# Performance work log

Hardware: AMD Instinct MI355X
Metric: run time of the kernel (lower is better)

Reference implementation:

```python
import jax, jax.numpy as jnp
import numpy as np


def lstm(xs, Wk, Wr, b, return_seq):
    # xs: (B, T, Din); Keras gate order i, f, c(g), o
    B = xs.shape[0]
    H = Wr.shape[0]

    def step(carry, x_t):
        h, c = carry
        z = x_t @ Wk + h @ Wr + b  # (B, 4H)
        i, f, g, o = jnp.split(z, 4, axis=-1)
        i = jax.nn.sigmoid(i)
        f = jax.nn.sigmoid(f)
        g = jnp.tanh(g)
        o = jax.nn.sigmoid(o)
        c = f * c + i * g
        h = o * jnp.tanh(c)
        return (h, c), h

    h0 = jnp.zeros((B, H), xs.dtype)
    (h, _), hs = jax.lax.scan(step, (h0, h0), jnp.swapaxes(xs, 0, 1))
    return jnp.swapaxes(hs, 0, 1) if return_seq else h


def setup_inputs() -> dict:
    key = jax.random.key(0)
    ks = jax.random.split(key, 10)
    B, T, F, H, P, O = 8192, 20, 8, 256, 15, 2
    s = 0.05
    return {
        "x": jax.random.normal(ks[0], (B, T, F), jnp.float32),
        "w_in_k": jax.random.normal(ks[1], (F, 64), jnp.float32) * s,
        "w_in_b": jnp.zeros((64,), jnp.float32),
        "enc_k": jax.random.normal(ks[2], (64, 4 * H), jnp.float32) * s,
        "enc_rk": jax.random.normal(ks[3], (H, 4 * H), jnp.float32) * s,
        "enc_b": jnp.zeros((4 * H,), jnp.float32),
        "dec_k": jax.random.normal(ks[4], (H, 4 * H), jnp.float32) * s,
        "dec_rk": jax.random.normal(ks[5], (H, 4 * H), jnp.float32) * s,
        "dec_b": jnp.zeros((4 * H,), jnp.float32),
        "mean_k": jax.random.normal(ks[6], (H, O), jnp.float32) * s,
        "mean_b": jnp.zeros((O,), jnp.float32),
        "lv_k": jax.random.normal(ks[7], (H, O), jnp.float32) * s,
        "lv_b": jnp.zeros((O,), jnp.float32),
    }


def reference(x, w_in_k, w_in_b, enc_k, enc_rk, enc_b,
              dec_k, dec_rk, dec_b, mean_k, mean_b, lv_k, lv_b):
    NUM_PRED = 15
    # input projection: Dense(64, relu)
    h = jax.nn.relu(x @ w_in_k + w_in_b)          # (B, T, 64)
    enc = lstm(h, enc_k, enc_rk, enc_b, False)    # (B, 256) last state
    rep = jnp.repeat(enc[:, None, :], NUM_PRED, axis=1)  # RepeatVector
    dec = lstm(rep, dec_k, dec_rk, dec_b, True)   # (B, 15, 256)
    mean = dec @ mean_k + mean_b                  # (B, 15, 2)
    log_var = jax.nn.relu(dec @ lv_k + lv_b)      # (B, 15, 2)
    return jnp.concatenate([mean, log_var], axis=-1)  # (B, 15, 4)
```

## Files before the change

kernel.cpp:

```cpp
#include <hip/hip_runtime.h>

#define TT 20
#define FF 8
#define HH 256
#define PP 15
#define DP 64
#define ROWS 32
#define NTHR 512
#define NBLK 256

typedef __attribute__((ext_vector_type(8))) _Float16 hfrag;
typedef __attribute__((ext_vector_type(16))) float f32x16;
typedef __attribute__((ext_vector_type(4))) float f32x4;

__device__ __forceinline__ int sw(int row, int k, int w){
  return (row * w + k) ^ ((row & 7) << 3);
}
__device__ __forceinline__ f32x16 zero16(){
  f32x16 v;
  #pragma unroll
  for (int i = 0; i < 16; ++i) v[i] = 0.f;
  return v;
}

__global__ void wprep(const float* __restrict__ ek, const float* __restrict__ erk,
                      const float* __restrict__ dk, const float* __restrict__ drk,
                      _Float16* __restrict__ ws){
  int i = blockIdx.x * 256 + threadIdx.x;
  const float* src; _Float16* dst; int ksh, rel;
  if (i < 4096)        { src = ek;  ksh = 2; rel = i;          dst = ws;           }
  else if (i < 20480)  { src = erk; ksh = 4; rel = i - 4096;   dst = ws + 65536;   }
  else if (i < 36864)  { src = dk;  ksh = 4; rel = i - 20480;  dst = ws + 327680;  }
  else                 { src = drk; ksh = 4; rel = i - 36864;  dst = ws + 589824;  }
  int lcol = rel & 31;
  int gkc  = rel >> 5;
  int kc   = gkc & ((1 << ksh) - 1);
  int wg   = gkc >> ksh;
  int g    = wg & 3, wid = wg >> 2;
  int col  = g * 256 + wid * 32 + lcol;
  int base = gkc * 512;
  #pragma unroll
  for (int lkh = 0; lkh < 2; ++lkh){
    _Float16 hbuf[8];
    #pragma unroll
    for (int e = 0; e < 8; ++e){
      int k = kc * 16 + lkh * 8 + e;
      hbuf[e] = (_Float16)src[k * 1024 + col];
    }
    int off = base + (lkh * 32 + lcol) * 8;
    *reinterpret_cast<hfrag*>(&dst[off]) = *reinterpret_cast<hfrag*>(hbuf);
  }
}

#define MM_STEPA(ACC, HSRC, WT, KD, NKC)                                                     \
  { const _Float16* ph = (WT) + (wid * 4 * (NKC)) * 512 + lane * 8;                          \
    _Pragma("unroll 4")                                                                      \
    for (int kc = 0; kc < (NKC); ++kc){                                                      \
      int k0 = kc * 16 + lkh * 8;                                                            \
      hfrag a = *reinterpret_cast<const hfrag*>(&(HSRC)[sw(lcol, k0, (KD))]);                \
      _Pragma("unroll")                                                                      \
      for (int g = 0; g < 4; ++g){                                                           \
        hfrag b = *reinterpret_cast<const hfrag*>(ph + (g * (NKC) + kc) * 512);              \
        ACC[g] = __builtin_amdgcn_mfma_f32_32x32x16_f16(a, b, ACC[g], 0, 0, 0);              \
      }                                                                                      \
    }                                                                                        \
  }

#define GATE_UPDATE(HDST, B0, B1, B2, B3, DOZERO)                                            \
  { _Pragma("unroll")                                                                        \
    for (int rg = 0; rg < 16; ++rg){                                                         \
      float zi = acc[0][rg] + (B0);                                                          \
      float zf = acc[1][rg] + (B1);                                                          \
      float zg = acc[2][rg] + (B2);                                                          \
      float zo = acc[3][rg] + (B3);                                                          \
      float ei = __expf(-zi), ef = __expf(-zf), eo = __expf(-zo);                            \
      float eg = __expf(2.f * zg);                                                           \
      float r1 = __builtin_amdgcn_rcpf(1.f + ef);                                            \
      float r2 = __builtin_amdgcn_rcpf((1.f + ei) * (eg + 1.f));                             \
      float cv = cst[rg] * r1 + (eg - 1.f) * r2;                        \
      cst[rg] = cv;                                                                          \
      float ec = __expf(2.f * cv);                                                           \
      float r3 = __builtin_amdgcn_rcpf((1.f + eo) * (ec + 1.f));                             \
      float hv = (ec - 1.f) * r3;                                             \
      int row = (rg & 3) + 8 * (rg >> 2) + 4 * lkh;                                          \
      (HDST)[sw(row, j, HH)] = (_Float16)hv;                                                 \
    }                                                                                        \
    if (DOZERO){ _Pragma("unroll") for (int g = 0; g < 4; ++g) acc[g] = zero16(); }          \
  }

#define STAGE_XP(tt, buf)                                                                    \
  { _Pragma("unroll")                                                                        \
    for (int rr = 0; rr < 4; ++rr){                                                          \
      int row = rb + 8 * rr;                                                                 \
      const float* xr = x + ((long)(r0 + row) * TT + (tt)) * FF;                             \
      f32x4 xa = *reinterpret_cast<const f32x4*>(xr);                                        \
      f32x4 xv = *reinterpret_cast<const f32x4*>(xr + 4);                                    \
      float s = bwin;                                                                        \
      _Pragma("unroll")                                                                      \
      for (int f = 0; f < 4; ++f){                                                           \
        s += xa[f] * winK[f * DP + xc];                                                      \
        s += xv[f] * winK[(f + 4) * DP + xc];                                                \
      }                                                                                      \
      s = fmaxf(s, 0.f);                                                                     \
      xb[buf][sw(row, xc, DP)] = (_Float16)s;                                                \
    } }

#define OUT_HEAD(tt)                                                                         \
  { float s = 0.f;                                                                           \
    _Pragma("unroll")                                                                        \
    for (int kb = 0; kb < 8; ++kb){                                                          \
      int k0 = sub_o * 64 + kb * 8;                                                          \
      hfrag vh = *reinterpret_cast<const hfrag*>(&h2[sw(orow_o, k0, HH)]);                   \
      _Pragma("unroll")                                                                      \
      for (int q = 0; q < 8; ++q){                                                           \
        s += (float)vh[q] * whead[(k0 + q) * 4 + ooc_o];                                     \
      }                                                                                      \
    }                                                                                        \
    s += __shfl_xor(s, 4);                                                                   \
    s += __shfl_xor(s, 8);                                                                   \
    if (sub_o == 0){                                                                         \
      s += hbias;                                                                            \
      if (ooc_o >= 2) s = fmaxf(s, 0.f);                                                     \
      out[(long)(r0 + orow_o) * (PP * 4) + (tt) * 4 + ooc_o] = s;                            \
    } }

__global__ __launch_bounds__(NTHR, 1) void lstm_main(
    const float* __restrict__ x,
    const float* __restrict__ w_in_k,
    const float* __restrict__ w_in_b,
    const float* __restrict__ enc_b,
    const float* __restrict__ dec_b,
    const float* __restrict__ mean_k,
    const float* __restrict__ mean_b,
    const float* __restrict__ lv_k,
    const float* __restrict__ lv_b,
    const _Float16* __restrict__ ws,
    float* __restrict__ out)
{
  __shared__ _Float16 h1[ROWS * HH];
  __shared__ _Float16 h2[ROWS * HH];
  __shared__ _Float16 xb[2][ROWS * DP];
  __shared__ float winK[FF * DP];
  __shared__ float whead[HH * 4];

  const int tid  = threadIdx.x;
  const int wid  = tid >> 6;
  const int lane = tid & 63;
  const int lcol = lane & 31;
  const int lkh  = lane >> 5;
  const int j    = wid * 32 + lcol;
  const int r0   = blockIdx.x * ROWS;

  const _Float16* enckT  = ws;
  const _Float16* encrkT = ws + 65536;
  const _Float16* deckT  = ws + 327680;
  const _Float16* decrkT = ws + 589824;

  if (tid < FF * DP) winK[tid] = w_in_k[tid];
  if (tid >= 256){
    int k = tid - 256;
    whead[k * 4 + 0] = mean_k[k * 2 + 0];
    whead[k * 4 + 1] = mean_k[k * 2 + 1];
    whead[k * 4 + 2] = lv_k[k * 2 + 0];
    whead[k * 4 + 3] = lv_k[k * 2 + 1];
  }

  const int xc = tid & 63;
  const int rb = tid >> 6;
  const float bwin = w_in_b[xc];

  const int orow_o = tid >> 4;
  const int sub_o  = (tid >> 2) & 3;
  const int ooc_o  = tid & 3;
  const float hbias = (ooc_o < 2) ? mean_b[ooc_o] : lv_b[ooc_o - 2];

  const float eb0 = enc_b[0 * HH + j], eb1 = enc_b[1 * HH + j];
  const float eb2 = enc_b[2 * HH + j], eb3 = enc_b[3 * HH + j];
  const float db0 = dec_b[0 * HH + j], db1 = dec_b[1 * HH + j];
  const float db2 = dec_b[2 * HH + j], db3 = dec_b[3 * HH + j];

  f32x16 acc[4];
  f32x16 accD[4];
  float  cst[16];
  #pragma unroll
  for (int g = 0; g < 4; ++g) acc[g] = zero16();
  #pragma unroll
  for (int r = 0; r < 16; ++r) cst[r] = 0.f;

  __syncthreads();
  STAGE_XP(0, 0);
  __syncthreads();

  for (int t = 0; t < TT; ++t){
    MM_STEPA(acc, xb[t & 1], enckT, DP, 4);
    if (t > 0){
      MM_STEPA(acc, h1, encrkT, HH, 16);
    }
    if (t + 1 < TT) STAGE_XP(t + 1, (t + 1) & 1);
    __syncthreads();
    GATE_UPDATE(h1, eb0, eb1, eb2, eb3, 1);
    __syncthreads();
  }

  #pragma unroll
  for (int g = 0; g < 4; ++g) accD[g] = zero16();
  {
    f32x16* acc = accD;
    MM_STEPA(acc, h1, deckT, HH, 16);
  }
  #pragma unroll
  for (int r = 0; r < 16; ++r) cst[r] = 0.f;

  for (int t = 0; t < PP; ++t){
    if (t > 0) OUT_HEAD(t - 1);
    #pragma unroll
    for (int g = 0; g < 4; ++g) acc[g] = accD[g];
    if (t > 0){
      MM_STEPA(acc, h2, decrkT, HH, 16);
    }
    __syncthreads();
    GATE_UPDATE(h2, db0, db1, db2, db3, 0);
    __syncthreads();
  }
  OUT_HEAD(PP - 1);
}

extern "C" void kernel_launch(void* const* d_in, const int* in_sizes, int n_in,
                              void* d_out, int out_size, void* d_ws, size_t ws_size,
                              hipStream_t stream)
{
  const float* x      = (const float*)d_in[0];
  const float* w_in_k = (const float*)d_in[1];
  const float* w_in_b = (const float*)d_in[2];
  const float* enc_k  = (const float*)d_in[3];
  const float* enc_rk = (const float*)d_in[4];
  const float* enc_b  = (const float*)d_in[5];
  const float* dec_k  = (const float*)d_in[6];
  const float* dec_rk = (const float*)d_in[7];
  const float* dec_b  = (const float*)d_in[8];
  const float* mean_k = (const float*)d_in[9];
  const float* mean_b = (const float*)d_in[10];
  const float* lv_k   = (const float*)d_in[11];
  const float* lv_b   = (const float*)d_in[12];
  _Float16* ws        = (_Float16*)d_ws;

  if (ws_size < 1703936) return;

  wprep<<<dim3(208), dim3(256), 0, stream>>>(enc_k, enc_rk, dec_k, dec_rk, ws);
  lstm_main<<<dim3(NBLK), dim3(NTHR), 0, stream>>>(x, w_in_k, w_in_b, enc_b, dec_b,
                                                   mean_k, mean_b, lv_k, lv_b, ws,
                                                   (float*)d_out);
}
```

Measured before the change: 366.8 us.

## Stream LSTM weight fragments through LDS ring with async global_load_lds prefetch

Replaces direct global loads of the fp16 weight fragments in the MFMA loops with a per-wave LDS ring buffer filled by global_load_lds, kept a fixed depth ahead of the consuming MFMA across timesteps and across the encoder/decoder boundary. It also swaps __syncthreads for raw s_waitcnt+s_barrier and moves the output head after the recurrent matmul. The aim is to hide global/L2 latency on weight reads. In exchange it adds LDS use and relies on hand-set vmcnt waits whose ordering must match the issue sequence exactly, and the decoder tail issues loads that are never consumed.

```diff
diff --git a/kernel.cpp b/kernel.cpp
--- a/kernel.cpp
+++ b/kernel.cpp
@@ -8,6 +8,8 @@
 #define ROWS 32
 #define NTHR 512
 #define NBLK 256
+#define RING 12
+#define DEPTH 10
 
 typedef __attribute__((ext_vector_type(8))) _Float16 hfrag;
 typedef __attribute__((ext_vector_type(16))) float f32x16;
@@ -22,6 +24,9 @@
   for (int i = 0; i < 16; ++i) v[i] = 0.f;
   return v;
 }
+
+#define BARRIER() asm volatile("s_waitcnt lgkmcnt(0)\n\ts_barrier" ::: "memory")
+#define WAITVM() asm volatile("s_waitcnt vmcnt(9)" ::: "memory")
 
 __global__ void wprep(const float* __restrict__ ek, const float* __restrict__ erk,
                       const float* __restrict__ dk, const float* __restrict__ drk,
@@ -52,19 +57,38 @@
   }
 }
 
-#define MM_STEPA(ACC, HSRC, WT, KD, NKC)                                                     \
-  { const _Float16* ph = (WT) + (wid * 4 * (NKC)) * 512 + lane * 8;                          \
-    _Pragma("unroll 4")                                                                      \
-    for (int kc = 0; kc < (NKC); ++kc){                                                      \
-      int k0 = kc * 16 + lkh * 8;                                                            \
-      hfrag a = *reinterpret_cast<const hfrag*>(&(HSRC)[sw(lcol, k0, (KD))]);                \
-      _Pragma("unroll")                                                                      \
-      for (int g = 0; g < 4; ++g){                                                           \
-        hfrag b = *reinterpret_cast<const hfrag*>(ph + (g * (NKC) + kc) * 512);              \
-        ACC[g] = __builtin_amdgcn_mfma_f32_32x32x16_f16(a, b, ACC[g], 0, 0, 0);              \
-      }                                                                                      \
-    }                                                                                        \
-  }
+#define PREISSUE(SRCEXPR)                                                                    \
+  { const _Float16* gsrc_ = (SRCEXPR);                                                       \
+    __builtin_amdgcn_global_load_lds(                                                        \
+        (const __attribute__((address_space(1))) unsigned int*)gsrc_,                        \
+        (__attribute__((address_space(3))) unsigned int*)&wring[wid][is][0], 16, 0, 0);      \
+    is = (is + 1 == RING) ? 0 : is + 1; }
+
+#define CONSUME_MFMA(A, ACCG, SRCEXPR)                                                       \
+  { WAITVM();                                                                                \
+    hfrag b_ = *reinterpret_cast<const hfrag*>(&wring[wid][cs][lane * 8]);                   \
+    cs = (cs + 1 == RING) ? 0 : cs + 1;                                                      \
+    PREISSUE(SRCEXPR);                                                                       \
+    ACCG = __builtin_amdgcn_mfma_f32_32x32x16_f16(A, b_, ACCG, 0, 0, 0); }
+
+__device__ __forceinline__ const _Float16* t0s(int lc, const _Float16* EKW){
+  int r = lc & 15;
+  return EKW + ((r & 3) * 4 + (r >> 2)) * 512;
+}
+__device__ __forceinline__ const _Float16* encs(int lc, int last, const _Float16* EKW,
+                                                const _Float16* RKW, const _Float16* DKW){
+  if (lc < 16) return EKW + ((lc & 3) * 4 + (lc >> 2)) * 512;
+  if (lc < 80){ int r = lc - 16; return RKW + ((r & 3) * 16 + (r >> 2)) * 512; }
+  int r = lc - 80;
+  return last ? DKW + ((r & 3) * 16 + (r >> 2)) * 512
+              : EKW + ((r & 3) * 4  + (r >> 2)) * 512;
+}
+__device__ __forceinline__ const _Float16* dks(int lc, const _Float16* DKW,
+                                               const _Float16* DRW){
+  if (lc < 64) return DKW + ((lc & 3) * 16 + (lc >> 2)) * 512;
+  int r = lc - 64;
+  return DRW + ((r & 3) * 16 + (r >> 2)) * 512;
+}
 
 #define GATE_UPDATE(HDST, B0, B1, B2, B3, DOZERO)                                            \
   { _Pragma("unroll")                                                                        \
@@ -140,6 +164,7 @@
   __shared__ _Float16 h1[ROWS * HH];
   __shared__ _Float16 h2[ROWS * HH];
   __shared__ _Float16 xb[2][ROWS * DP];
+  __shared__ _Float16 wring[8][RING][512];
   __shared__ float winK[FF * DP];
   __shared__ float whead[HH * 4];
 
@@ -151,10 +176,10 @@
   const int j    = wid * 32 + lcol;
   const int r0   = blockIdx.x * ROWS;
 
-  const _Float16* enckT  = ws;
-  const _Float16* encrkT = ws + 65536;
-  const _Float16* deckT  = ws + 327680;
-  const _Float16* decrkT = ws + 589824;
+  const _Float16* EKW = ws           + wid * 16 * 512 + lane * 8;
+  const _Float16* RKW = (ws + 65536) + wid * 64 * 512 + lane * 8;
+  const _Float16* DKW = (ws + 327680)+ wid * 64 * 512 + lane * 8;
+  const _Float16* DRW = (ws + 589824)+ wid * 64 * 512 + lane * 8;
 
   if (tid < FF * DP) winK[tid] = w_in_k[tid];
   if (tid >= 256){
@@ -187,40 +212,81 @@
   #pragma unroll
   for (int r = 0; r < 16; ++r) cst[r] = 0.f;
 
-  __syncthreads();
+  int cs = 0, is = 0;
+
+  #pragma unroll
+  for (int c = 0; c < DEPTH; ++c) PREISSUE(t0s(c, EKW));
+
   STAGE_XP(0, 0);
-  __syncthreads();
-
-  for (int t = 0; t < TT; ++t){
-    MM_STEPA(acc, xb[t & 1], enckT, DP, 4);
-    if (t > 0){
-      MM_STEPA(acc, h1, encrkT, HH, 16);
+  BARRIER();
+
+  #pragma unroll
+  for (int kc = 0; kc < 4; ++kc){
+    hfrag a = *reinterpret_cast<const hfrag*>(&xb[0][sw(lcol, kc * 16 + lkh * 8, DP)]);
+    CONSUME_MFMA(a, acc[0], t0s(kc * 4 + 0 + DEPTH, EKW));
+    CONSUME_MFMA(a, acc[1], t0s(kc * 4 + 1 + DEPTH, EKW));
+    CONSUME_MFMA(a, acc[2], t0s(kc * 4 + 2 + DEPTH, EKW));
+    CONSUME_MFMA(a, acc[3], t0s(kc * 4 + 3 + DEPTH, EKW));
+  }
+  STAGE_XP(1, 1);
+  GATE_UPDATE(h1, eb0, eb1, eb2, eb3, 1);
+  BARRIER();
+
+  for (int t = 1; t < TT; ++t){
+    const int last = (t == TT - 1);
+    #pragma unroll
+    for (int kc = 0; kc < 4; ++kc){
+      hfrag a = *reinterpret_cast<const hfrag*>(&xb[t & 1][sw(lcol, kc * 16 + lkh * 8, DP)]);
+      CONSUME_MFMA(a, acc[0], encs(kc * 4 + 0 + DEPTH, last, EKW, RKW, DKW));
+      CONSUME_MFMA(a, acc[1], encs(kc * 4 + 1 + DEPTH, last, EKW, RKW, DKW));
+      CONSUME_MFMA(a, acc[2], encs(kc * 4 + 2 + DEPTH, last, EKW, RKW, DKW));
+      CONSUME_MFMA(a, acc[3], encs(kc * 4 + 3 + DEPTH, last, EKW, RKW, DKW));
     }
+    #pragma unroll 4
+    for (int kc = 0; kc < 16; ++kc){
+      hfrag a = *reinterpret_cast<const hfrag*>(&h1[sw(lcol, kc * 16 + lkh * 8, HH)]);
+      CONSUME_MFMA(a, acc[0], encs(16 + kc * 4 + 0 + DEPTH, last, EKW, RKW, DKW));
+      CONSUME_MFMA(a, acc[1], encs(16 + kc * 4 + 1 + DEPTH, last, EKW, RKW, DKW));
+      CONSUME_MFMA(a, acc[2], encs(16 + kc * 4 + 2 + DEPTH, last, EKW, RKW, DKW));
+      CONSUME_MFMA(a, acc[3], encs(16 + kc * 4 + 3 + DEPTH, last, EKW, RKW, DKW));
+    }
+    BARRIER();
     if (t + 1 < TT) STAGE_XP(t + 1, (t + 1) & 1);
-    __syncthreads();
     GATE_UPDATE(h1, eb0, eb1, eb2, eb3, 1);
-    __syncthreads();
+    BARRIER();
   }
 
   #pragma unroll
   for (int g = 0; g < 4; ++g) accD[g] = zero16();
-  {
-    f32x16* acc = accD;
-    MM_STEPA(acc, h1, deckT, HH, 16);
+  #pragma unroll 4
+  for (int kc = 0; kc < 16; ++kc){
+    hfrag a = *reinterpret_cast<const hfrag*>(&h1[sw(lcol, kc * 16 + lkh * 8, HH)]);
+    CONSUME_MFMA(a, accD[0], dks(kc * 4 + 0 + DEPTH, DKW, DRW));
+    CONSUME_MFMA(a, accD[1], dks(kc * 4 + 1 + DEPTH, DKW, DRW));
+    CONSUME_MFMA(a, accD[2], dks(kc * 4 + 2 + DEPTH, DKW, DRW));
+    CONSUME_MFMA(a, accD[3], dks(kc * 4 + 3 + DEPTH, DKW, DRW));
   }
   #pragma unroll
   for (int r = 0; r < 16; ++r) cst[r] = 0.f;
 
   for (int t = 0; t < PP; ++t){
-    if (t > 0) OUT_HEAD(t - 1);
     #pragma unroll
     for (int g = 0; g < 4; ++g) acc[g] = accD[g];
     if (t > 0){
-      MM_STEPA(acc, h2, decrkT, HH, 16);
+      #pragma unroll 4
+      for (int kc = 0; kc < 16; ++kc){
+        hfrag a = *reinterpret_cast<const hfrag*>(&h2[sw(lcol, kc * 16 + lkh * 8, HH)]);
+        int c0 = kc * 4;
+        CONSUME_MFMA(a, acc[0], DRW + ((((c0+0+DEPTH)&63) & 3) * 16 + (((c0+0+DEPTH)&63) >> 2)) * 512);
+        CONSUME_MFMA(a, acc[1], DRW + ((((c0+1+DEPTH)&63) & 3) * 16 + (((c0+1+DEPTH)&63) >> 2)) * 512);
+        CONSUME_MFMA(a, acc[2], DRW + ((((c0+2+DEPTH)&63) & 3) * 16 + (((c0+2+DEPTH)&63) >> 2)) * 512);
+        CONSUME_MFMA(a, acc[3], DRW + ((((c0+3+DEPTH)&63) & 3) * 16 + (((c0+3+DEPTH)&63) >> 2)) * 512);
+      }
+      OUT_HEAD(t - 1);
+      BARRIER();
     }
-    __syncthreads();
     GATE_UPDATE(h2, db0, db1, db2, db3, 0);
-    __syncthreads();
+    BARRIER();
   }
   OUT_HEAD(PP - 1);
 }
```

Measured after the change: 546.5 us. 1.49x slower.
